# Kernel optimization log

Measured on AMD Instinct MI355X. Metric: run time of the kernel, lower is better.

Reference implementation:

```python
import jax, jax.numpy as jnp
import numpy as np

B, H, W, DIM = 16, 64, 64, 512
GH, GW = 8, 8
NH = 16
HD = DIM // NH
POS = DIM // 16  # DynamicPosBias pos_dim = (dim//4)//4 = 32
EPS = 1e-5


def setup_inputs() -> dict:
    key = jax.random.key(0)
    ks = jax.random.split(key, 12)
    w = lambda k, s: jax.random.normal(k, s, jnp.float32) * 0.02
    f32 = jnp.float32
    return {
        "x": jax.random.normal(ks[0], (B, H * W, DIM), f32),
        "norm1_g": jnp.ones((DIM,), f32), "norm1_b": jnp.zeros((DIM,), f32),
        "qkv_w": w(ks[1], (3 * DIM, DIM)), "qkv_b": jnp.zeros((3 * DIM,), f32),
        "proj_w": w(ks[2], (DIM, DIM)), "proj_b": jnp.zeros((DIM,), f32),
        "pos_w0": w(ks[3], (POS, 2)), "pos_b0": jnp.zeros((POS,), f32),
        "pos_ln0_g": jnp.ones((POS,), f32), "pos_ln0_b": jnp.zeros((POS,), f32),
        "pos_w1": w(ks[4], (POS, POS)), "pos_b1": jnp.zeros((POS,), f32),
        "pos_ln1_g": jnp.ones((POS,), f32), "pos_ln1_b": jnp.zeros((POS,), f32),
        "pos_w2": w(ks[5], (POS, POS)), "pos_b2": jnp.zeros((POS,), f32),
        "pos_ln2_g": jnp.ones((POS,), f32), "pos_ln2_b": jnp.zeros((POS,), f32),
        "pos_w3": w(ks[6], (NH, POS)), "pos_b3": jnp.zeros((NH,), f32),
        "norm2_g": jnp.ones((DIM,), f32), "norm2_b": jnp.zeros((DIM,), f32),
        "mlp_w1": w(ks[7], (4 * DIM, DIM)), "mlp_b1": jnp.zeros((4 * DIM,), f32),
        "mlp_w2": w(ks[8], (DIM, 4 * DIM)), "mlp_b2": jnp.zeros((DIM,), f32),
    }


def _ln(x, g, b):
    m = jnp.mean(x, -1, keepdims=True)
    v = jnp.mean(jnp.square(x - m), -1, keepdims=True)
    return (x - m) * jax.lax.rsqrt(v + EPS) * g + b


def _rel_bias_tables():
    # relative coordinate table [(2GH-1)*(2GW-1), 2]
    ph = jnp.arange(1 - GH, GH)
    pw = jnp.arange(1 - GW, GW)
    biases = jnp.stack(jnp.meshgrid(ph, pw, indexing="ij")).reshape(2, -1).T.astype(jnp.float32)
    # relative position index [GH*GW, GH*GW]
    coords = jnp.stack(jnp.meshgrid(jnp.arange(GH), jnp.arange(GW), indexing="ij")).reshape(2, -1)
    rel = (coords[:, :, None] - coords[:, None, :]).transpose(1, 2, 0)  # [N,N,2]
    idx = (rel[..., 0] + GH - 1) * (2 * GW - 1) + (rel[..., 1] + GW - 1)
    return biases, idx


def reference(x, norm1_g, norm1_b, qkv_w, qkv_b, proj_w, proj_b,
              pos_w0, pos_b0, pos_ln0_g, pos_ln0_b,
              pos_w1, pos_b1, pos_ln1_g, pos_ln1_b,
              pos_w2, pos_b2, pos_ln2_g, pos_ln2_b,
              pos_w3, pos_b3, norm2_g, norm2_b,
              mlp_w1, mlp_b1, mlp_w2, mlp_b2):
    biases, rel_idx = _rel_bias_tables()
    Ng = GH * GW
    scale = HD ** -0.5

    shortcut = x
    h = _ln(x, norm1_g, norm1_b).reshape(B, H, W, DIM)
    # use_lda=True: long-distance (strided) grouping
    h = h.reshape(B, GH, H // GH, GW, W // GW, DIM).transpose(0, 2, 4, 1, 3, 5)
    h = h.reshape(B * (H * W) // Ng, Ng, DIM)  # [G, Ng, C]

    # attention
    qkv = h @ qkv_w.T + qkv_b
    qkv = qkv.reshape(-1, Ng, 3, NH, HD).transpose(2, 0, 3, 1, 4)  # [3,G,NH,Ng,HD]
    q, k, v = qkv[0], qkv[1], qkv[2]
    attn = jnp.einsum("ghnd,ghmd->ghnm", q * scale, k)

    # dynamic position bias MLP on the coordinate table
    p = jax.nn.relu(_ln(biases @ pos_w0.T + pos_b0, pos_ln0_g, pos_ln0_b))
    p = jax.nn.relu(_ln(p @ pos_w1.T + pos_b1, pos_ln1_g, pos_ln1_b))
    p = jax.nn.relu(_ln(p @ pos_w2.T + pos_b2, pos_ln2_g, pos_ln2_b))
    p = p @ pos_w3.T + pos_b3  # [(2GH-1)(2GW-1), NH]
    rel_bias = p[rel_idx].transpose(2, 0, 1)  # [NH, Ng, Ng]

    attn = jax.nn.softmax(attn + rel_bias[None], axis=-1)
    o = jnp.einsum("ghnm,ghmd->ghnd", attn, v)
    o = o.transpose(0, 2, 1, 3).reshape(-1, Ng, DIM)
    o = o @ proj_w.T + proj_b

    # ungroup (inverse of lda grouping)
    o = o.reshape(B, H // GH, W // GW, GH, GW, DIM)
    o = o.transpose(0, 3, 1, 4, 2, 5).reshape(B, H * W, DIM)

    x = shortcut + o
    m = _ln(x, norm2_g, norm2_b)
    m = jax.nn.gelu(m @ mlp_w1.T + mlp_b1, approximate=False)
    m = m @ mlp_w2.T + mlp_b2
    return x + m
```

## Files before the change

### kernel.cpp

```cpp
#include <hip/hip_runtime.h>
#include <hip/hip_bf16.h>

typedef __bf16 bf16;
typedef __bf16 bf16x8 __attribute__((ext_vector_type(8)));
typedef __bf16 bf16x4 __attribute__((ext_vector_type(4)));
typedef float f32x4_t __attribute__((ext_vector_type(4)));

static constexpr int kDIM = 512;

static constexpr size_t OFF_QKVW = 0;
static constexpr size_t OFF_PROJW = 1572864;
static constexpr size_t OFF_W1   = 2097152;
static constexpr size_t OFF_W2   = 4194304;
static constexpr size_t OFF_PTAB = 6291456;
static constexpr size_t OFF_A    = 8388608;
static constexpr size_t OFF_B    = 276824064;

typedef __attribute__((address_space(3))) uint32_t lds_u32_t;
typedef __attribute__((address_space(1))) const uint32_t glb_u32_t;
#define ASYNC_COPY16(gp, lp) __builtin_amdgcn_global_load_lds((glb_u32_t*)(gp), (lds_u32_t*)(lp), 16, 0, 0)
#define WAITV0() asm volatile("s_waitcnt vmcnt(0)" ::: "memory")

__global__ void cast_fp8_k(const float* __restrict__ in, unsigned char* __restrict__ out, int n4)
{
    int i = blockIdx.x * blockDim.x + threadIdx.x;
    if (i < n4) {
        float4 v = ((const float4*)in)[i];
        int p = __builtin_amdgcn_cvt_pk_fp8_f32(v.x * 64.0f, v.y * 64.0f, 0, false);
        p = __builtin_amdgcn_cvt_pk_fp8_f32(v.z * 64.0f, v.w * 64.0f, p, true);
        ((unsigned int*)out)[i] = (unsigned int)p;
    }
}

__global__ void cast_fp8_perm_k(const float* __restrict__ in, unsigned char* __restrict__ out,
                                int n4, int ncols)
{
    int i = blockIdx.x * blockDim.x + threadIdx.x;
    if (i < n4) {
        float4 v = ((const float4*)in)[i];
        int idx = i * 4;
        int row = idx / ncols;
        int j0 = idx - row * ncols;
        float vv[4] = {v.x, v.y, v.z, v.w};
#pragma unroll
        for (int t = 0; t < 4; ++t) {
            int j = j0 + t;
            int pj = (j & ~127) | (j & 64) | ((j & 15) << 2) | ((j >> 4) & 3);
            int p8 = __builtin_amdgcn_cvt_pk_fp8_f32(vv[t] * 64.0f, vv[t] * 64.0f, 0, false);
            out[(size_t)row * ncols + pj] = (unsigned char)(p8 & 0xff);
        }
    }
}

template<int GROUP>
__global__ __launch_bounds__(256)
void ln_k(const float* __restrict__ x, const float* __restrict__ gw,
          const float* __restrict__ bw, unsigned char* __restrict__ out)
{
    const int t = blockIdx.x * 4 + (threadIdx.x >> 6);
    const int lane = threadIdx.x & 63;
    const float* xp = x + (size_t)t * kDIM + lane * 8;
    float4 p0 = *(const float4*)xp;
    float4 p1 = *(const float4*)(xp + 4);
    float v[8] = {p0.x, p0.y, p0.z, p0.w, p1.x, p1.y, p1.z, p1.w};
    float s = 0.f;
#pragma unroll
    for (int i = 0; i < 8; ++i) s += v[i];
#pragma unroll
    for (int off = 32; off > 0; off >>= 1) s += __shfl_xor(s, off);
    const float mean = s * (1.0f / 512.0f);
    float q = 0.f;
#pragma unroll
    for (int i = 0; i < 8; ++i) { float d = v[i] - mean; q += d * d; }
#pragma unroll
    for (int off = 32; off > 0; off >>= 1) q += __shfl_xor(q, off);
    const float rstd = rsqrtf(q * (1.0f / 512.0f) + 1e-5f);
    size_t orow;
    if (GROUP) {
        int b = t >> 12, r = (t >> 6) & 63, c = t & 63;
        int g = b * 64 + (r & 7) * 8 + (c & 7);
        int n = (r >> 3) * 8 + (c >> 3);
        orow = (size_t)g * 64 + n;
    } else {
        orow = t;
    }
    float4 g0 = *(const float4*)(gw + lane * 8);
    float4 g1 = *(const float4*)(gw + lane * 8 + 4);
    float4 b0 = *(const float4*)(bw + lane * 8);
    float4 b1 = *(const float4*)(bw + lane * 8 + 4);
    float gg[8] = {g0.x, g0.y, g0.z, g0.w, g1.x, g1.y, g1.z, g1.w};
    float bb[8] = {b0.x, b0.y, b0.z, b0.w, b1.x, b1.y, b1.z, b1.w};
    float o[8];
#pragma unroll
    for (int i = 0; i < 8; ++i) o[i] = ((v[i] - mean) * rstd * gg[i] + bb[i]) * 32.0f;
    unsigned int lo = 0, hi = 0;
    lo = (unsigned int)__builtin_amdgcn_cvt_pk_fp8_f32(o[0], o[1], 0, false);
    lo = (unsigned int)__builtin_amdgcn_cvt_pk_fp8_f32(o[2], o[3], (int)lo, true);
    hi = (unsigned int)__builtin_amdgcn_cvt_pk_fp8_f32(o[4], o[5], 0, false);
    hi = (unsigned int)__builtin_amdgcn_cvt_pk_fp8_f32(o[6], o[7], (int)hi, true);
    uint2 u; u.x = lo; u.y = hi;
    *(uint2*)(out + orow * kDIM + lane * 8) = u;
}

__device__ inline void ln32_relu(float* h, const float* g, const float* b)
{
    float m = 0.f;
#pragma unroll
    for (int i = 0; i < 32; ++i) m += h[i];
    m *= (1.0f / 32.0f);
    float v = 0.f;
#pragma unroll
    for (int i = 0; i < 32; ++i) { float d = h[i] - m; v += d * d; }
    v *= (1.0f / 32.0f);
    float r = rsqrtf(v + 1e-5f);
#pragma unroll
    for (int i = 0; i < 32; ++i) h[i] = fmaxf((h[i] - m) * r * g[i] + b[i], 0.f);
}

__global__ __launch_bounds__(256)
void posmlp_k(const float* __restrict__ w0, const float* __restrict__ b0,
              const float* __restrict__ g0, const float* __restrict__ bb0,
              const float* __restrict__ w1, const float* __restrict__ b1,
              const float* __restrict__ g1, const float* __restrict__ bb1,
              const float* __restrict__ w2, const float* __restrict__ b2,
              const float* __restrict__ g2, const float* __restrict__ bb2,
              const float* __restrict__ w3, const float* __restrict__ b3,
              float* __restrict__ ptab)
{
    int r = threadIdx.x;
    if (r >= 225) return;
    float in0 = (float)(r / 15) - 7.0f;
    float in1 = (float)(r % 15) - 7.0f;
    float h[32], h2[32];
#pragma unroll
    for (int o = 0; o < 32; ++o) h[o] = w0[o * 2] * in0 + w0[o * 2 + 1] * in1 + b0[o];
    ln32_relu(h, g0, bb0);
#pragma unroll
    for (int o = 0; o < 32; ++o) {
        float s = b1[o];
#pragma unroll
        for (int i = 0; i < 32; ++i) s += w1[o * 32 + i] * h[i];
        h2[o] = s;
    }
    ln32_relu(h2, g1, bb1);
#pragma unroll
    for (int o = 0; o < 32; ++o) {
        float s = b2[o];
#pragma unroll
        for (int i = 0; i < 32; ++i) s += w2[o * 32 + i] * h2[i];
        h[o] = s;
    }
    ln32_relu(h, g2, bb2);
#pragma unroll
    for (int o = 0; o < 16; ++o) {
        float s = b3[o];
#pragma unroll
        for (int i = 0; i < 32; ++i) s += w3[o * 32 + i] * h[i];
        ptab[r * 16 + o] = s;
    }
}

__global__ __launch_bounds__(256)
void attn_mfma_k(const unsigned char* __restrict__ qkv, const float* __restrict__ ptab,
                 unsigned char* __restrict__ obuf)
{
    const int g  = blockIdx.x >> 1;
    const int hb = blockIdx.x & 1;
    const int w  = threadIdx.x >> 6;
    const int lane = threadIdx.x & 63;
    const int c = lane & 15, q = lane >> 4;

    __shared__ float ptl[16][240];
    __shared__ alignas(16) bf16 pl[4][4096];
    __shared__ alignas(16) bf16 vt[4][2048];

    for (int i = threadIdx.x; i < 3600; i += 256)
        ptl[i & 15][i >> 4] = ptab[i];
    __syncthreads();

    const size_t rowb = (size_t)g * 64;
    bf16* pw = pl[w];
    char* vw = (char*)vt[w];

    for (int hh = 0; hh < 2; ++hh) {
        const int head = hb * 8 + hh * 4 + w;
        const unsigned char* qb = qkv + rowb * 2048 + head * 32;

        const bf16* vbase = (const bf16*)(qb + 1024 + head * 32);
        bf16x8 vrow[4];
#pragma unroll
        for (int l = 0; l < 4; ++l)
            vrow[l] = *(const bf16x8*)((const bf16*)((const char*)vbase + (size_t)lane * 2048) + l * 8);

        long aq[4], bk[4];
#pragma unroll
        for (int i = 0; i < 4; ++i) {
            aq[i] = *(const long*)(qb + (size_t)(i * 16 + c) * 2048 + q * 8);
            bk[i] = *(const long*)(qb + 512 + (size_t)(i * 16 + c) * 2048 + q * 8);
        }

        f32x4_t s[4][4];
#pragma unroll
        for (int i = 0; i < 4; ++i)
#pragma unroll
            for (int j = 0; j < 4; ++j)
                s[i][j] = __builtin_amdgcn_mfma_f32_16x16x32_fp8_fp8(aq[i], bk[j],
                          (f32x4_t){0.f, 0.f, 0.f, 0.f}, 0, 0, 0);

#pragma unroll
        for (int l = 0; l < 4; ++l)
#pragma unroll
            for (int j = 0; j < 8; ++j) {
                const int d = l * 8 + j;
                *(bf16*)(vw + d * 128 + ((lane * 2) ^ ((d & 7) << 4))) = vrow[l][j];
            }

        const float scale = 0.17677669529663687f / 1024.0f;
        float inv[4][4];
#pragma unroll
        for (int i = 0; i < 4; ++i)
#pragma unroll
            for (int jj = 0; jj < 4; ++jj) {
                const int n = i * 16 + q * 4 + jj;
                const int na = n >> 3, nu = n & 7;
                float mx = -1e30f;
#pragma unroll
                for (int j = 0; j < 4; ++j) {
                    const int m = j * 16 + c;
                    const int idx = (na - (m >> 3) + 7) * 15 + (nu - (m & 7) + 7);
                    float v = s[i][j][jj] * scale + ptl[head][idx];
                    s[i][j][jj] = v;
                    mx = fmaxf(mx, v);
                }
#pragma unroll
                for (int off = 1; off < 16; off <<= 1) mx = fmaxf(mx, __shfl_xor(mx, off));
                float sum = 0.f;
#pragma unroll
                for (int j = 0; j < 4; ++j) {
                    float e = __expf(s[i][j][jj] - mx);
                    s[i][j][jj] = e; sum += e;
                }
#pragma unroll
                for (int off = 1; off < 16; off <<= 1) sum += __shfl_xor(sum, off);
                inv[i][jj] = 1.0f / sum;
            }

#pragma unroll
        for (int i = 0; i < 4; ++i)
#pragma unroll
            for (int jj = 0; jj < 4; ++jj) {
                const int n = i * 16 + q * 4 + jj;
                const int swz = (n & 7) << 4;
#pragma unroll
                for (int j = 0; j < 4; ++j) {
                    const int m = j * 16 + c;
                    *(bf16*)((char*)pw + n * 128 + ((m * 2) ^ swz)) = (bf16)s[i][j][jj];
                }
            }

        bf16x8 bv[2][2];
#pragma unroll
        for (int ks = 0; ks < 2; ++ks)
#pragma unroll
            for (int dt = 0; dt < 2; ++dt)
                bv[ks][dt] = *(const bf16x8*)(vw + (dt * 16 + c) * 128 +
                              ((ks * 64 + q * 16) ^ ((c & 7) << 4)));

        f32x4_t o[4][2];
#pragma unroll
        for (int i = 0; i < 4; ++i)
#pragma unroll
            for (int dt = 0; dt < 2; ++dt)
                o[i][dt] = (f32x4_t){0.f, 0.f, 0.f, 0.f};
#pragma unroll
        for (int ks = 0; ks < 2; ++ks)
#pragma unroll
            for (int i = 0; i < 4; ++i) {
                const int n = i * 16 + c;
                bf16x8 ap = *(const bf16x8*)((char*)pw + n * 128 +
                             ((ks * 64 + q * 16) ^ ((n & 7) << 4)));
#pragma unroll
                for (int dt = 0; dt < 2; ++dt)
                    o[i][dt] = __builtin_amdgcn_mfma_f32_16x16x32_bf16(ap, bv[ks][dt], o[i][dt], 0, 0, 0);
            }

        unsigned char* ob = obuf + rowb * 512 + head * 32;
#pragma unroll
        for (int i = 0; i < 4; ++i)
#pragma unroll
            for (int dt = 0; dt < 2; ++dt)
#pragma unroll
                for (int jj = 0; jj < 4; ++jj) {
                    const int n = i * 16 + q * 4 + jj;
                    float val = o[i][dt][jj] * inv[i][jj] * 32.0f;
                    int p8 = __builtin_amdgcn_cvt_pk_fp8_f32(val, val, 0, false);
                    ob[(size_t)n * 512 + dt * 16 + c] = (unsigned char)(p8 & 0xff);
                }
    }
}

template<int MODE, int NBX, int K>
__global__ __launch_bounds__(256, 2)
void gemm_fp8(const unsigned char* __restrict__ A, const unsigned char* __restrict__ Bw,
              const float* __restrict__ bias, const float* __restrict__ resid,
              void* __restrict__ outp, int N, float invs)
{
    __shared__ alignas(16) unsigned char As[128 * 128];
    __shared__ alignas(16) unsigned char Bs[128 * 128];
    const int tid = threadIdx.x;
    const int lane = tid & 63;
    const int w = tid >> 6;
    const int wr = w >> 1, wc = w & 1;
    const int c = lane & 15, q = lane >> 4;

    const int bid = blockIdx.y * NBX + blockIdx.x;
    const int nwg = gridDim.y * NBX;
    const int swz = (bid & 7) * (nwg >> 3) + (bid >> 3);
    const int by = swz / NBX;
    const int bx = swz - by * NBX;
    const int rowBase = by * 128;
    const int colBase = bx * 128;

    f32x4_t acc[4][4];
#pragma unroll
    for (int m = 0; m < 4; ++m)
#pragma unroll
        for (int n = 0; n < 4; ++n)
            acc[m][n] = (f32x4_t){0.f, 0.f, 0.f, 0.f};

    const int key = c & 7;
    const int hb8 = (q & 1) * 8;

    const int sg = (tid & 7) ^ ((tid >> 3) & 7);
    const unsigned char* aBase = A + (size_t)(rowBase + (tid >> 3)) * K + sg * 16;
    const unsigned char* bBase = Bw + (size_t)(colBase + (tid >> 3)) * K + sg * 16;
    unsigned char* ldsA = As + (tid & 192) * 16;
    unsigned char* ldsB = Bs + (tid & 192) * 16;

#pragma unroll 2
    for (int kt = 0; kt < K; kt += 128) {
#pragma unroll
        for (int l = 0; l < 4; ++l) {
            ASYNC_COPY16(aBase + (size_t)l * 32 * K + kt, ldsA + l * 4096);
            ASYNC_COPY16(bBase + (size_t)l * 32 * K + kt, ldsB + l * 4096);
        }
        WAITV0();
        __syncthreads();
#pragma unroll
        for (int kk = 0; kk < 4; ++kk) {
            const int sb = (((2 * kk + (q >> 1)) ^ key) << 4) + hb8;
            long af[4], bfr[4];
#pragma unroll
            for (int m = 0; m < 4; ++m) {
                const int row = wr * 64 + m * 16 + c;
                af[m] = *(const long*)((const char*)As + row * 128 + sb);
            }
#pragma unroll
            for (int n = 0; n < 4; ++n) {
                const int row = wc * 64 + n * 16 + c;
                bfr[n] = *(const long*)((const char*)Bs + row * 128 + sb);
            }
#pragma unroll
            for (int m = 0; m < 4; ++m)
#pragma unroll
                for (int n = 0; n < 4; ++n)
                    acc[m][n] = __builtin_amdgcn_mfma_f32_16x16x32_fp8_fp8(af[m], bfr[n], acc[m][n], 0, 0, 0);
        }
        __syncthreads();
    }

#pragma unroll
    for (int m = 0; m < 4; ++m) {
#pragma unroll
        for (int jj = 0; jj < 4; ++jj) {
            int grow = rowBase + wr * 64 + m * 16 + q * 4 + jj;
            float vv[4];
#pragma unroll
            for (int n = 0; n < 4; ++n)
                vv[n] = acc[m][n][jj] * invs + bias[colBase + wc * 64 + n * 16 + c];
            if constexpr (MODE == 0) {
                char* ob = (char*)outp;
                if (colBase < 1024) {
                    int p0 = __builtin_amdgcn_cvt_pk_fp8_f32(vv[0] * 32.0f, vv[1] * 32.0f, 0, false);
                    int p1 = __builtin_amdgcn_cvt_pk_fp8_f32(vv[2] * 32.0f, vv[3] * 32.0f, 0, false);
                    *(unsigned short*)(ob + (size_t)grow * 2048 + colBase + wc * 64 + c * 2) =
                        (unsigned short)(p0 & 0xffff);
                    *(unsigned short*)(ob + (size_t)grow * 2048 + colBase + wc * 64 + 32 + c * 2) =
                        (unsigned short)(p1 & 0xffff);
                } else {
#pragma unroll
                    for (int n = 0; n < 4; ++n) {
                        int gcol = colBase + wc * 64 + n * 16 + c;
                        *(bf16*)(ob + (size_t)grow * 2048 + 1024 + (size_t)(gcol - 1024) * 2) = (bf16)vv[n];
                    }
                }
            } else if constexpr (MODE == 1) {
#pragma unroll
                for (int n = 0; n < 4; ++n) {
                    float v = vv[n];
                    float e = __expf(1.5957691216057308f * (v + 0.044715f * v * v * v));
                    vv[n] = v * (e / (1.0f + e)) * 64.0f;
                }
                int p = __builtin_amdgcn_cvt_pk_fp8_f32(vv[0], vv[1], 0, false);
                p = __builtin_amdgcn_cvt_pk_fp8_f32(vv[2], vv[3], p, true);
                *(unsigned int*)((char*)outp + (size_t)grow * N + colBase + wc * 64 + c * 4) =
                    (unsigned int)p;
            } else {
#pragma unroll
                for (int n = 0; n < 4; ++n) {
                    int gcol = colBase + wc * 64 + n * 16 + c;
                    float v = vv[n];
                    if constexpr (MODE == 2) {
                        int g = grow >> 6, ns = grow & 63;
                        int b = g >> 6, i = (g >> 3) & 7, j = g & 7;
                        int a = ns >> 3, u = ns & 7;
                        int t = b * 4096 + (a * 8 + i) * 64 + (u * 8 + j);
                        size_t oi = (size_t)t * 512 + gcol;
                        ((float*)outp)[oi] = resid[oi] + v;
                    } else {
                        size_t oi = (size_t)grow * 512 + gcol;
                        ((float*)outp)[oi] = resid[oi] + v;
                    }
                }
            }
        }
    }
}

extern "C" void kernel_launch(void* const* d_in, const int* in_sizes, int n_in,
                              void* d_out, int out_size, void* d_ws, size_t ws_size,
                              hipStream_t stream)
{
    const float* x    = (const float*)d_in[0];
    const float* n1g  = (const float*)d_in[1];
    const float* n1b  = (const float*)d_in[2];
    const float* qkvw = (const float*)d_in[3];
    const float* qkvb = (const float*)d_in[4];
    const float* pjw  = (const float*)d_in[5];
    const float* pjb  = (const float*)d_in[6];
    const float* pw0  = (const float*)d_in[7];
    const float* pb0  = (const float*)d_in[8];
    const float* pg0  = (const float*)d_in[9];
    const float* pbb0 = (const float*)d_in[10];
    const float* pw1  = (const float*)d_in[11];
    const float* pb1  = (const float*)d_in[12];
    const float* pg1  = (const float*)d_in[13];
    const float* pbb1 = (const float*)d_in[14];
    const float* pw2  = (const float*)d_in[15];
    const float* pb2  = (const float*)d_in[16];
    const float* pg2  = (const float*)d_in[17];
    const float* pbb2 = (const float*)d_in[18];
    const float* pw3  = (const float*)d_in[19];
    const float* pb3  = (const float*)d_in[20];
    const float* n2g  = (const float*)d_in[21];
    const float* n2b  = (const float*)d_in[22];
    const float* w1   = (const float*)d_in[23];
    const float* b1   = (const float*)d_in[24];
    const float* w2   = (const float*)d_in[25];
    const float* b2   = (const float*)d_in[26];

    char* ws = (char*)d_ws;
    unsigned char* qkvw_f8 = (unsigned char*)(ws + OFF_QKVW);
    unsigned char* pjw_f8  = (unsigned char*)(ws + OFF_PROJW);
    unsigned char* w1_f8 = (unsigned char*)(ws + OFF_W1);
    unsigned char* w2_f8 = (unsigned char*)(ws + OFF_W2);
    float* ptab  = (float*)(ws + OFF_PTAB);
    unsigned char* bufA8 = (unsigned char*)(ws + OFF_A);
    unsigned char* bufB8 = (unsigned char*)(ws + OFF_B);
    float* xout  = (float*)d_out;

    cast_fp8_k<<<(1536 * 512 / 4 + 255) / 256, 256, 0, stream>>>(qkvw, qkvw_f8, 1536 * 512 / 4);
    cast_fp8_k<<<(512 * 512 / 4 + 255) / 256, 256, 0, stream>>>(pjw, pjw_f8, 512 * 512 / 4);
    cast_fp8_k<<<(2048 * 512 / 4 + 255) / 256, 256, 0, stream>>>(w1, w1_f8, 2048 * 512 / 4);
    cast_fp8_perm_k<<<(512 * 2048 / 4 + 255) / 256, 256, 0, stream>>>(w2, w2_f8, 512 * 2048 / 4, 2048);

    posmlp_k<<<1, 256, 0, stream>>>(pw0, pb0, pg0, pbb0, pw1, pb1, pg1, pbb1,
                                    pw2, pb2, pg2, pbb2, pw3, pb3, ptab);

    ln_k<1><<<16384, 256, 0, stream>>>(x, n1g, n1b, bufB8);

    gemm_fp8<0, 12, 512><<<dim3(12, 512), 256, 0, stream>>>(bufB8, qkvw_f8, qkvb, nullptr,
                                                            bufA8, 1536, 1.0f / 2048.0f);

    attn_mfma_k<<<2048, 256, 0, stream>>>(bufA8, ptab, bufB8);

    gemm_fp8<2, 4, 512><<<dim3(4, 512), 256, 0, stream>>>(bufB8, pjw_f8, pjb, x,
                                                          xout, 512, 1.0f / 2048.0f);

    ln_k<0><<<16384, 256, 0, stream>>>(xout, n2g, n2b, bufB8);

    gemm_fp8<1, 16, 512><<<dim3(16, 512), 256, 0, stream>>>(bufB8, w1_f8, b1, nullptr,
                                                            bufA8, 2048, 1.0f / 2048.0f);

    gemm_fp8<3, 4, 2048><<<dim3(4, 512), 256, 0, stream>>>(bufA8, w2_f8, b2, xout,
                                                           xout, 512, 1.0f / 4096.0f);
}
```

Measured before the change: 657.1 us.

## Pack V bf16 stores, permute proj weights, use fast division

Measured after the change: 663.1 us (median of 2 runs). No clear change (+0.9%).

```diff
diff --git a/kernel.cpp b/kernel.cpp
--- a/kernel.cpp
+++ b/kernel.cpp
@@ -46,6 +46,26 @@
         for (int t = 0; t < 4; ++t) {
             int j = j0 + t;
             int pj = (j & ~127) | (j & 64) | ((j & 15) << 2) | ((j >> 4) & 3);
+            int p8 = __builtin_amdgcn_cvt_pk_fp8_f32(vv[t] * 64.0f, vv[t] * 64.0f, 0, false);
+            out[(size_t)row * ncols + pj] = (unsigned char)(p8 & 0xff);
+        }
+    }
+}
+
+__global__ void cast_fp8_permv_k(const float* __restrict__ in, unsigned char* __restrict__ out,
+                                 int n4, int ncols)
+{
+    int i = blockIdx.x * blockDim.x + threadIdx.x;
+    if (i < n4) {
+        float4 v = ((const float4*)in)[i];
+        int idx = i * 4;
+        int row = idx / ncols;
+        int j0 = idx - row * ncols;
+        float vv[4] = {v.x, v.y, v.z, v.w};
+#pragma unroll
+        for (int t = 0; t < 4; ++t) {
+            int j = j0 + t;
+            int pj = (j & ~31) | ((j & 15) << 1) | ((j >> 4) & 1);
             int p8 = __builtin_amdgcn_cvt_pk_fp8_f32(vv[t] * 64.0f, vv[t] * 64.0f, 0, false);
             out[(size_t)row * ncols + pj] = (unsigned char)(p8 & 0xff);
         }
@@ -242,7 +262,7 @@
                 }
 #pragma unroll
                 for (int off = 1; off < 16; off <<= 1) sum += __shfl_xor(sum, off);
-                inv[i][jj] = 1.0f / sum;
+                inv[i][jj] = __fdividef(1.0f, sum);
             }
 
 #pragma unroll
@@ -388,18 +408,21 @@
                     *(unsigned short*)(ob + (size_t)grow * 2048 + colBase + wc * 64 + 32 + c * 2) =
                         (unsigned short)(p1 & 0xffff);
                 } else {
-#pragma unroll
-                    for (int n = 0; n < 4; ++n) {
-                        int gcol = colBase + wc * 64 + n * 16 + c;
-                        *(bf16*)(ob + (size_t)grow * 2048 + 1024 + (size_t)(gcol - 1024) * 2) = (bf16)vv[n];
-                    }
+                    bf16 t0 = (bf16)vv[0], t1 = (bf16)vv[1], t2 = (bf16)vv[2], t3 = (bf16)vv[3];
+                    unsigned int pk0 = ((unsigned int)*(unsigned short*)&t1 << 16) |
+                                       (unsigned int)*(unsigned short*)&t0;
+                    unsigned int pk1 = ((unsigned int)*(unsigned short*)&t3 << 16) |
+                                       (unsigned int)*(unsigned short*)&t2;
+                    size_t vb = (size_t)grow * 2048 + 1024 + (size_t)(colBase - 1024 + wc * 64) * 2;
+                    *(unsigned int*)(ob + vb + c * 4) = pk0;
+                    *(unsigned int*)(ob + vb + 64 + c * 4) = pk1;
                 }
             } else if constexpr (MODE == 1) {
 #pragma unroll
                 for (int n = 0; n < 4; ++n) {
                     float v = vv[n];
                     float e = __expf(1.5957691216057308f * (v + 0.044715f * v * v * v));
-                    vv[n] = v * (e / (1.0f + e)) * 64.0f;
+                    vv[n] = v * __fdividef(e, 1.0f + e) * 64.0f;
                 }
                 int p = __builtin_amdgcn_cvt_pk_fp8_f32(vv[0], vv[1], 0, false);
                 p = __builtin_amdgcn_cvt_pk_fp8_f32(vv[2], vv[3], p, true);
@@ -470,7 +493,7 @@
     float* xout  = (float*)d_out;
 
     cast_fp8_k<<<(1536 * 512 / 4 + 255) / 256, 256, 0, stream>>>(qkvw, qkvw_f8, 1536 * 512 / 4);
-    cast_fp8_k<<<(512 * 512 / 4 + 255) / 256, 256, 0, stream>>>(pjw, pjw_f8, 512 * 512 / 4);
+    cast_fp8_permv_k<<<(512 * 512 / 4 + 255) / 256, 256, 0, stream>>>(pjw, pjw_f8, 512 * 512 / 4, 512);
     cast_fp8_k<<<(2048 * 512 / 4 + 255) / 256, 256, 0, stream>>>(w1, w1_f8, 2048 * 512 / 4);
     cast_fp8_perm_k<<<(512 * 2048 / 4 + 255) / 256, 256, 0, stream>>>(w2, w2_f8, 512 * 2048 / 4, 2048);
 
```
